# Performance work log

Measured on AMD Instinct MI355X. Metric: run time of the kernel, lower is better.

The kernel has to match this reference:

```python
import jax, jax.numpy as jnp
import numpy as np

B, S_LEN, H_LEN, DIM = 2048, 64, 256, 256
NULL_ATT = -float(2 ** 22)


def setup_inputs() -> dict:
    key = jax.random.key(0)
    k1, k2, k3, k4, k5, k6, k7 = jax.random.split(key, 7)
    return {
        "item_emb": jax.random.normal(k1, (B, DIM), dtype=jnp.float32),
        "x_session": jax.random.normal(k2, (B, S_LEN, DIM), dtype=jnp.float32),
        "session_len": jax.random.randint(k3, (B,), 0, S_LEN, dtype=jnp.int32),
        "user_hist": jax.random.normal(k4, (B, H_LEN, DIM), dtype=jnp.float32),
        "hist_len": jax.random.randint(k5, (B,), 0, H_LEN, dtype=jnp.int32),
        "W1": jax.random.normal(k6, (DIM, 2 * DIM), dtype=jnp.float32) * 0.05,
        "b1": jax.random.normal(k7, (DIM,), dtype=jnp.float32) * 0.05,
    }


def reference(item_emb, x_session, session_len, user_hist, hist_len, W1, b1):
    # item_emb [B,d], x_session [B,s,d], user_hist [B,h,d]
    batch, s_len, dim = x_session.shape
    h_len = user_hist.shape[1]
    # fc1 query does not depend on history position -> compute once per (b,s)
    q_in = jnp.concatenate(
        [jnp.broadcast_to(item_emb[:, None, :], x_session.shape), x_session], axis=-1
    )  # [B,s,2d]
    query = q_in @ W1.T + b1  # [B,s,d]
    # attention scores: sum over dim of hist * query for every (s,h) pair
    att = jnp.einsum("bsd,bhd->bsh", query, user_hist)  # [B,s,h]
    mask_s = (jnp.arange(s_len)[None, :] < session_len[:, None])[:, :, None]
    mask_h = (jnp.arange(h_len)[None, :] < hist_len[:, None])[:, None, :]
    att = jnp.where(mask_s & mask_h, att, jnp.float32(NULL_ATT))
    score = jnp.max(att, axis=1)  # max over session positions -> [B,h]
    w = jax.nn.softmax(score, axis=1)  # [B,h]
    user_hist_rep = jnp.sum(user_hist * w[:, :, None], axis=1)  # [B,d]
    return user_hist_rep, score
```

## Files before the change

### kernel.cpp

```cpp
#include <hip/hip_runtime.h>

#define NB 2048
#define NULL_ATT (-4194304.0f)

typedef __attribute__((ext_vector_type(8))) _Float16 f16x8;
typedef __attribute__((ext_vector_type(2))) _Float16 h2;
typedef __attribute__((ext_vector_type(4))) float f32x4;

__device__ __align__(16) short g_wxf16[256 * 256];
__device__ float g_iq[NB * 256];

__device__ __forceinline__ int qoff(int s, int k) {
    int g = k >> 3;
    return s * 256 + (((g ^ (s & 7)) << 3) | (k & 7));
}

__device__ __forceinline__ f16x8 cvt8h(float4 a, float4 b) {
    f16x8 r;
    r[0] = (_Float16)a.x; r[1] = (_Float16)a.y; r[2] = (_Float16)a.z; r[3] = (_Float16)a.w;
    r[4] = (_Float16)b.x; r[5] = (_Float16)b.y; r[6] = (_Float16)b.z; r[7] = (_Float16)b.w;
    return r;
}

__device__ __forceinline__ void stage8(const float* __restrict__ p, f16x8 dst[8]) {
    float4 r[8][2];
    #pragma unroll
    for (int kc = 0; kc < 8; ++kc) {
        r[kc][0] = *(const float4*)(p + kc * 32);
        r[kc][1] = *(const float4*)(p + kc * 32 + 4);
    }
    #pragma unroll
    for (int kc = 0; kc < 8; ++kc) dst[kc] = cvt8h(r[kc][0], r[kc][1]);
}

__global__ __launch_bounds__(256, 4) void prep(const float* __restrict__ item_emb,
                                               const float* __restrict__ W1,
                                               const float* __restrict__ b1) {
    if (blockIdx.x < 256) {
        int j = blockIdx.x, k = threadIdx.x;
        g_wxf16[j * 256 + k] =
            __builtin_bit_cast(short, (_Float16)W1[(size_t)j * 512 + 256 + k]);
        return;
    }
    const int m0 = (blockIdx.x - 256) * 16;
    const int t = threadIdx.x, wave = t >> 6, lane = t & 63;
    const int lr = lane & 15, lo8 = lane >> 4;
    const int jb = wave * 64;

    f16x8 afr[8];
    stage8(item_emb + (size_t)(m0 + lr) * 256 + lo8 * 8, afr);

    f32x4 acc[4];
    #pragma unroll
    for (int jt = 0; jt < 4; ++jt) acc[jt] = f32x4{0.f, 0.f, 0.f, 0.f};
    #pragma unroll
    for (int kc = 0; kc < 8; ++kc) {
        #pragma unroll
        for (int jt = 0; jt < 4; ++jt) {
            const float* wp = W1 + (size_t)(jb + jt * 16 + lr) * 512 + kc * 32 + lo8 * 8;
            f16x8 bfr = cvt8h(*(const float4*)wp, *(const float4*)(wp + 4));
            acc[jt] = __builtin_amdgcn_mfma_f32_16x16x32_f16(afr[kc], bfr, acc[jt], 0, 0, 0);
        }
    }
    #pragma unroll
    for (int jt = 0; jt < 4; ++jt) {
        float bv = b1[jb + jt * 16 + lr];
        #pragma unroll
        for (int i = 0; i < 4; ++i)
            g_iq[(size_t)(m0 + lo8 * 4 + i) * 256 + jb + jt * 16 + lr] = acc[jt][i] + bv;
    }
}

#define AA_GET(i) (h2{parr[(i) >> 2][(((i) & 3) << 1)], parr[(i) >> 2][(((i) & 3) << 1) | 1]})
#define AA_SET(i, v) { parr[(i) >> 2][(((i) & 3) << 1)] = (v)[0]; \
                       parr[(i) >> 2][(((i) & 3) << 1) | 1] = (v)[1]; }

__global__ __launch_bounds__(256, 4) void coatt_main(
    const float* __restrict__ x_session,
    const int*   __restrict__ session_len,
    const float* __restrict__ user_hist,
    const int*   __restrict__ hist_len,
    float* __restrict__ out)
{
    const int b = blockIdx.x;
    const int t = threadIdx.x;
    const int wave = t >> 6;
    const int lane = t & 63;
    const int lr  = lane & 15;
    const int lo8 = lane >> 4;
    const int sl = session_len[b];
    const int hl = hist_len[b];

    __shared__ __align__(16) short qf[64 * 256];
    __shared__ float sMax[256];
    __shared__ float red2[8];
    __shared__ __align__(16) float Vp[4][256];

    sMax[t] = NULL_ATT;
    const int nst = (sl > 0) ? min(4, (sl + 15) >> 4) : 0;

    if (wave < nst) {
        const int st = wave;
        f16x8 afr[8];
        stage8(x_session + ((size_t)b * 64 + st * 16 + lr) * 256 + lo8 * 8, afr);

        #pragma unroll
        for (int jc = 0; jc < 4; ++jc) {
            f32x4 acc[4];
            #pragma unroll
            for (int jt = 0; jt < 4; ++jt) {
                float v = g_iq[(size_t)b * 256 + jc * 64 + jt * 16 + lr];
                acc[jt] = f32x4{v, v, v, v};
            }
            #pragma unroll
            for (int kc = 0; kc < 8; ++kc) {
                #pragma unroll
                for (int jt = 0; jt < 4; ++jt) {
                    f16x8 bfr2 = *(const f16x8*)&g_wxf16[(jc * 64 + jt * 16 + lr) * 256 + kc * 32 + lo8 * 8];
                    acc[jt] = __builtin_amdgcn_mfma_f32_16x16x32_f16(afr[kc], bfr2, acc[jt], 0, 0, 0);
                }
            }
            #pragma unroll
            for (int jt = 0; jt < 4; ++jt) {
                int j = jc * 64 + jt * 16 + lr;
                #pragma unroll
                for (int i = 0; i < 4; ++i)
                    qf[qoff(st * 16 + lo8 * 4 + i, j)] =
                        __builtin_bit_cast(short, (_Float16)acc[jt][i]);
            }
        }
    }

    const int nht = (hl + 15) >> 4;
    const bool p2 = (nst > 0 && hl > 0);
    const float* hB = user_hist + (size_t)b * 256 * 256;
    f16x8 bcur[8];
    if (p2 && wave < nht)
        stage8(hB + (size_t)(wave * 16 + lr) * 256 + lo8 * 8, bcur);
    __syncthreads();

    float Mrun = -3.0e38f;
    float Drun = 0.0f;
    f16x8 parr[8];
    #pragma unroll
    for (int kc = 0; kc < 8; ++kc) parr[kc] = f16x8{0, 0, 0, 0, 0, 0, 0, 0};

    if (p2) {
        for (int slot = 0; slot < 4; ++slot) {
            const int ht = wave + slot * 4;
            if (ht >= nht) break;
            if (slot > 0)
                stage8(hB + (size_t)(ht * 16 + lr) * 256 + lo8 * 8, bcur);

            f32x4 acc[4];
            #pragma unroll
            for (int st = 0; st < 4; ++st) acc[st] = f32x4{0.f, 0.f, 0.f, 0.f};
            #pragma unroll
            for (int kc = 0; kc < 8; ++kc) {
                #pragma unroll
                for (int st = 0; st < 4; ++st) {
                    if (st < nst) {
                        f16x8 a = *(const f16x8*)&qf[qoff(st * 16 + lr, kc * 32 + lo8 * 8)];
                        acc[st] = __builtin_amdgcn_mfma_f32_16x16x32_f16(a, bcur[kc], acc[st], 0, 0, 0);
                    }
                }
            }
            float m = NULL_ATT;
            #pragma unroll
            for (int st = 0; st < 4; ++st) {
                if (st < nst) {
                    #pragma unroll
                    for (int i = 0; i < 4; ++i) {
                        int s = st * 16 + lo8 * 4 + i;
                        if (s < sl) m = fmaxf(m, acc[st][i]);
                    }
                }
            }
            m = fmaxf(m, __shfl_xor(m, 16, 64));
            m = fmaxf(m, __shfl_xor(m, 32, 64));
            const int h = ht * 16 + lr;
            if (lane < 16 && h < hl) sMax[h] = m;

            float sh = (h < hl) ? m : NULL_ATT;
            float mt = sh;
            mt = fmaxf(mt, __shfl_xor(mt, 1, 64));
            mt = fmaxf(mt, __shfl_xor(mt, 2, 64));
            mt = fmaxf(mt, __shfl_xor(mt, 4, 64));
            mt = fmaxf(mt, __shfl_xor(mt, 8, 64));
            if (mt > Mrun) {
                float scl = __expf(Mrun - mt);
                Drun *= scl;
                const _Float16 s16 = (_Float16)scl;
                f16x8 s8 = {s16, s16, s16, s16, s16, s16, s16, s16};
                #pragma unroll
                for (int kc = 0; kc < 8; ++kc) parr[kc] *= s8;
                Mrun = mt;
            }
            float eh = __expf(sh - Mrun);
            Drun += eh;

            {
                const _Float16 e16 = (_Float16)eh;
                f16x8 e8 = {e16, e16, e16, e16, e16, e16, e16, e16};
                #pragma unroll
                for (int kc = 0; kc < 8; ++kc) parr[kc] = bcur[kc] * e8 + parr[kc];
            }
        }

        #pragma unroll
        for (int sb = 0; sb < 4; ++sb) {
            const int bmask = 8 >> sb;
            const int half = 16 >> sb;
            const bool hi = (lr & bmask) != 0;
            #pragma unroll
            for (int i = 0; i < (16 >> sb); ++i) {
                h2 a0 = AA_GET(i);
                h2 a1 = AA_GET(i + half);
                h2 keep = hi ? a1 : a0;
                h2 send = hi ? a0 : a1;
                int ru = __shfl_xor(__builtin_bit_cast(int, send), bmask, 64);
                h2 res = keep + __builtin_bit_cast(h2, ru);
                AA_SET(i, res);
            }
        }
        h2 f0 = AA_GET(0), f1 = AA_GET(1);

        float Dl = Drun;
        Dl += __shfl_xor(Dl, 1, 64);
        Dl += __shfl_xor(Dl, 2, 64);
        Dl += __shfl_xor(Dl, 4, 64);
        Dl += __shfl_xor(Dl, 8, 64);
        if (lane == 0) { red2[wave] = Mrun; red2[4 + wave] = Dl; }
        const int col0 = (lr >> 1) * 32 + lo8 * 8 + (lr & 1) * 4;
        *(float4*)&Vp[wave][col0] =
            float4{(float)f0[0], (float)f0[1], (float)f1[0], (float)f1[1]};
    }
    __syncthreads();

    float sc = sMax[t];
    out[(size_t)NB * 256 + (size_t)b * 256 + t] = sc;

    if (p2) {
        float M0 = red2[0], M1 = red2[1], M2 = red2[2], M3 = red2[3];
        float Ms = fmaxf(fmaxf(M0, M1), fmaxf(M2, M3));
        float w0 = __expf(M0 - Ms), w1 = __expf(M1 - Ms);
        float w2 = __expf(M2 - Ms), w3 = __expf(M3 - Ms);
        float denom = w0 * red2[4] + w1 * red2[5] + w2 * red2[6] + w3 * red2[7];
        float num = w0 * Vp[0][t] + w1 * Vp[1][t] + w2 * Vp[2][t] + w3 * Vp[3][t];
        out[(size_t)b * 256 + t] = num / denom;
    } else {
        f32x4 a4 = {0.f, 0.f, 0.f, 0.f};
        const float* hc = hB + lane * 4;
        for (int h = wave; h < 256; h += 16) {
            float4 v0 = *(const float4*)(hc + (size_t)(h)      * 256);
            float4 v1 = *(const float4*)(hc + (size_t)(h + 4)  * 256);
            float4 v2 = *(const float4*)(hc + (size_t)(h + 8)  * 256);
            float4 v3 = *(const float4*)(hc + (size_t)(h + 12) * 256);
            a4[0] += (v0.x + v1.x) + (v2.x + v3.x);
            a4[1] += (v0.y + v1.y) + (v2.y + v3.y);
            a4[2] += (v0.z + v1.z) + (v2.z + v3.z);
            a4[3] += (v0.w + v1.w) + (v2.w + v3.w);
        }
        *(float4*)&Vp[wave][lane * 4] = float4{a4[0], a4[1], a4[2], a4[3]};
        __syncthreads();
        out[(size_t)b * 256 + t] =
            ((Vp[0][t] + Vp[1][t]) + (Vp[2][t] + Vp[3][t])) * (1.0f / 256.0f);
    }
}

extern "C" void kernel_launch(void* const* d_in, const int* in_sizes, int n_in,
                              void* d_out, int out_size, void* d_ws, size_t ws_size,
                              hipStream_t stream) {
    const float* item_emb    = (const float*)d_in[0];
    const float* x_session   = (const float*)d_in[1];
    const int*   session_len = (const int*)d_in[2];
    const float* user_hist   = (const float*)d_in[3];
    const int*   hist_len    = (const int*)d_in[4];
    const float* W1          = (const float*)d_in[5];
    const float* b1          = (const float*)d_in[6];
    float* out = (float*)d_out;

    prep<<<384, 256, 0, stream>>>(item_emb, W1, b1);
    coatt_main<<<NB, 256, 0, stream>>>(x_session, session_len, user_hist, hist_len, out);
}
```

Before: 181.3 us.

## Double block to eight waves and split query and history work

The main kernel now launches 512 threads per batch row instead of 256. The query GEMM is split across wave pairs, each handling half the output columns, and each wave processes at most two history tiles instead of four. Staging loads are split into two half-loads to limit register pressure. The cross-wave softmax merge now combines 8 partial results, with the partial vectors stored in fp16 shared memory. This shortens the serial per-block chain at the cost of more register pressure under the tighter launch bounds, and adds some fp16 rounding in the partial sums.

After: 262.3 us. +44.7%, slower.

```diff
diff --git a/kernel.cpp b/kernel.cpp
--- a/kernel.cpp
+++ b/kernel.cpp
@@ -22,15 +22,19 @@
     return r;
 }
 
-__device__ __forceinline__ void stage8(const float* __restrict__ p, f16x8 dst[8]) {
-    float4 r[8][2];
-    #pragma unroll
-    for (int kc = 0; kc < 8; ++kc) {
+__device__ __forceinline__ void stage4(const float* __restrict__ p, f16x8* dst) {
+    float4 r[4][2];
+    #pragma unroll
+    for (int kc = 0; kc < 4; ++kc) {
         r[kc][0] = *(const float4*)(p + kc * 32);
         r[kc][1] = *(const float4*)(p + kc * 32 + 4);
     }
     #pragma unroll
-    for (int kc = 0; kc < 8; ++kc) dst[kc] = cvt8h(r[kc][0], r[kc][1]);
+    for (int kc = 0; kc < 4; ++kc) dst[kc] = cvt8h(r[kc][0], r[kc][1]);
+}
+__device__ __forceinline__ void stage8c(const float* __restrict__ p, f16x8 dst[8]) {
+    stage4(p, dst);
+    stage4(p + 128, dst + 4);
 }
 
 __global__ __launch_bounds__(256, 4) void prep(const float* __restrict__ item_emb,
@@ -48,7 +52,7 @@
     const int jb = wave * 64;
 
     f16x8 afr[8];
-    stage8(item_emb + (size_t)(m0 + lr) * 256 + lo8 * 8, afr);
+    stage8c(item_emb + (size_t)(m0 + lr) * 256 + lo8 * 8, afr);
 
     f32x4 acc[4];
     #pragma unroll
@@ -75,7 +79,7 @@
 #define AA_SET(i, v) { parr[(i) >> 2][(((i) & 3) << 1)] = (v)[0]; \
                        parr[(i) >> 2][(((i) & 3) << 1) | 1] = (v)[1]; }
 
-__global__ __launch_bounds__(256, 4) void coatt_main(
+__global__ __launch_bounds__(512, 8) void coatt_main(
     const float* __restrict__ x_session,
     const int*   __restrict__ session_len,
     const float* __restrict__ user_hist,
@@ -93,25 +97,33 @@
 
     __shared__ __align__(16) short qf[64 * 256];
     __shared__ float sMax[256];
-    __shared__ float red2[8];
-    __shared__ __align__(16) float Vp[4][256];
-
-    sMax[t] = NULL_ATT;
+    __shared__ float red2[16];
+    __shared__ __align__(8) h2 Vp[8][128];
+
+    if (t < 256) sMax[t] = NULL_ATT;
     const int nst = (sl > 0) ? min(4, (sl + 15) >> 4) : 0;
 
-    if (wave < nst) {
-        const int st = wave;
+    if ((wave & 3) < nst) {
+        const int st = wave & 3;
+        const int jh = wave >> 2;
+        float iqv[2][4];
+        #pragma unroll
+        for (int jc2 = 0; jc2 < 2; ++jc2) {
+            const int jc = jh * 2 + jc2;
+            #pragma unroll
+            for (int jt = 0; jt < 4; ++jt)
+                iqv[jc2][jt] = g_iq[(size_t)b * 256 + jc * 64 + jt * 16 + lr];
+        }
         f16x8 afr[8];
-        stage8(x_session + ((size_t)b * 64 + st * 16 + lr) * 256 + lo8 * 8, afr);
-
-        #pragma unroll
-        for (int jc = 0; jc < 4; ++jc) {
+        stage8c(x_session + ((size_t)b * 64 + st * 16 + lr) * 256 + lo8 * 8, afr);
+
+        #pragma unroll
+        for (int jc2 = 0; jc2 < 2; ++jc2) {
+            const int jc = jh * 2 + jc2;
             f32x4 acc[4];
             #pragma unroll
-            for (int jt = 0; jt < 4; ++jt) {
-                float v = g_iq[(size_t)b * 256 + jc * 64 + jt * 16 + lr];
-                acc[jt] = f32x4{v, v, v, v};
-            }
+            for (int jt = 0; jt < 4; ++jt)
+                acc[jt] = f32x4{iqv[jc2][jt], iqv[jc2][jt], iqv[jc2][jt], iqv[jc2][jt]};
             #pragma unroll
             for (int kc = 0; kc < 8; ++kc) {
                 #pragma unroll
@@ -136,7 +148,7 @@
     const float* hB = user_hist + (size_t)b * 256 * 256;
     f16x8 bcur[8];
     if (p2 && wave < nht)
-        stage8(hB + (size_t)(wave * 16 + lr) * 256 + lo8 * 8, bcur);
+        stage8c(hB + (size_t)(wave * 16 + lr) * 256 + lo8 * 8, bcur);
     __syncthreads();
 
     float Mrun = -3.0e38f;
@@ -146,12 +158,7 @@
     for (int kc = 0; kc < 8; ++kc) parr[kc] = f16x8{0, 0, 0, 0, 0, 0, 0, 0};
 
     if (p2) {
-        for (int slot = 0; slot < 4; ++slot) {
-            const int ht = wave + slot * 4;
-            if (ht >= nht) break;
-            if (slot > 0)
-                stage8(hB + (size_t)(ht * 16 + lr) * 256 + lo8 * 8, bcur);
-
+        auto slot_body = [&](int ht) {
             f32x4 acc[4];
             #pragma unroll
             for (int st = 0; st < 4; ++st) acc[st] = f32x4{0.f, 0.f, 0.f, 0.f};
@@ -198,13 +205,17 @@
             }
             float eh = __expf(sh - Mrun);
             Drun += eh;
-
-            {
-                const _Float16 e16 = (_Float16)eh;
-                f16x8 e8 = {e16, e16, e16, e16, e16, e16, e16, e16};
-                #pragma unroll
-                for (int kc = 0; kc < 8; ++kc) parr[kc] = bcur[kc] * e8 + parr[kc];
-            }
+            const _Float16 e16 = (_Float16)eh;
+            f16x8 e8 = {e16, e16, e16, e16, e16, e16, e16, e16};
+            #pragma unroll
+            for (int kc = 0; kc < 8; ++kc) parr[kc] = bcur[kc] * e8 + parr[kc];
+        };
+
+        if (wave < nht) slot_body(wave);
+        const int ht1 = wave + 8;
+        if (ht1 < nht) {
+            stage8c(hB + (size_t)(ht1 * 16 + lr) * 256 + lo8 * 8, bcur);
+            slot_body(ht1);
         }
 
         #pragma unroll
@@ -230,41 +241,43 @@
         Dl += __shfl_xor(Dl, 2, 64);
         Dl += __shfl_xor(Dl, 4, 64);
         Dl += __shfl_xor(Dl, 8, 64);
-        if (lane == 0) { red2[wave] = Mrun; red2[4 + wave] = Dl; }
+        if (lane == 0) { red2[wave] = Mrun; red2[8 + wave] = Dl; }
         const int col0 = (lr >> 1) * 32 + lo8 * 8 + (lr & 1) * 4;
-        *(float4*)&Vp[wave][col0] =
-            float4{(float)f0[0], (float)f0[1], (float)f1[0], (float)f1[1]};
-    }
-    __syncthreads();
-
-    float sc = sMax[t];
-    out[(size_t)NB * 256 + (size_t)b * 256 + t] = sc;
-
-    if (p2) {
-        float M0 = red2[0], M1 = red2[1], M2 = red2[2], M3 = red2[3];
-        float Ms = fmaxf(fmaxf(M0, M1), fmaxf(M2, M3));
-        float w0 = __expf(M0 - Ms), w1 = __expf(M1 - Ms);
-        float w2 = __expf(M2 - Ms), w3 = __expf(M3 - Ms);
-        float denom = w0 * red2[4] + w1 * red2[5] + w2 * red2[6] + w3 * red2[7];
-        float num = w0 * Vp[0][t] + w1 * Vp[1][t] + w2 * Vp[2][t] + w3 * Vp[3][t];
-        out[(size_t)b * 256 + t] = num / denom;
+        Vp[wave][col0 >> 1] = f0;
+        Vp[wave][(col0 >> 1) + 1] = f1;
     } else {
         f32x4 a4 = {0.f, 0.f, 0.f, 0.f};
         const float* hc = hB + lane * 4;
-        for (int h = wave; h < 256; h += 16) {
+        for (int h = wave; h < 256; h += 32) {
             float4 v0 = *(const float4*)(hc + (size_t)(h)      * 256);
-            float4 v1 = *(const float4*)(hc + (size_t)(h + 4)  * 256);
-            float4 v2 = *(const float4*)(hc + (size_t)(h + 8)  * 256);
-            float4 v3 = *(const float4*)(hc + (size_t)(h + 12) * 256);
+            float4 v1 = *(const float4*)(hc + (size_t)(h + 8)  * 256);
+            float4 v2 = *(const float4*)(hc + (size_t)(h + 16) * 256);
+            float4 v3 = *(const float4*)(hc + (size_t)(h + 24) * 256);
             a4[0] += (v0.x + v1.x) + (v2.x + v3.x);
             a4[1] += (v0.y + v1.y) + (v2.y + v3.y);
             a4[2] += (v0.z + v1.z) + (v2.z + v3.z);
             a4[3] += (v0.w + v1.w) + (v2.w + v3.w);
         }
-        *(float4*)&Vp[wave][lane * 4] = float4{a4[0], a4[1], a4[2], a4[3]};
-        __syncthreads();
-        out[(size_t)b * 256 + t] =
-            ((Vp[0][t] + Vp[1][t]) + (Vp[2][t] + Vp[3][t])) * (1.0f / 256.0f);
+        Vp[wave][lane * 2]     = h2{(_Float16)a4[0], (_Float16)a4[1]};
+        Vp[wave][lane * 2 + 1] = h2{(_Float16)a4[2], (_Float16)a4[3]};
+        if (lane == 0) { red2[wave] = 0.f; red2[8 + wave] = 32.f; }
+    }
+    __syncthreads();
+
+    if (t < 256) {
+        out[(size_t)NB * 256 + (size_t)b * 256 + t] = sMax[t];
+        float Ms = red2[0];
+        #pragma unroll
+        for (int w = 1; w < 8; ++w) Ms = fmaxf(Ms, red2[w]);
+        float num = 0.f, den = 0.f;
+        #pragma unroll
+        for (int w = 0; w < 8; ++w) {
+            float ww = __expf(red2[w] - Ms);
+            den += ww * red2[8 + w];
+            h2 v = Vp[w][t >> 1];
+            num += ww * (float)v[t & 1];
+        }
+        out[(size_t)b * 256 + t] = num / den;
     }
 }
 
@@ -281,5 +294,5 @@
     float* out = (float*)d_out;
 
     prep<<<384, 256, 0, stream>>>(item_emb, W1, b1);
-    coatt_main<<<NB, 256, 0, stream>>>(x_session, session_len, user_hist, hist_len, out);
-}
+    coatt_main<<<NB, 512, 0, stream>>>(x_session, session_len, user_hist, hist_len, out);
+}
```
